# Optimization experiments

Hardware: AMD Instinct MI355X
Metric: run time of the kernel (lower is better)

## Reference

```python
import jax, jax.numpy as jnp
import numpy as np

B, S, SV = 4, 2048, 50
QF = KF = VF = E = 1024
SCALE = np.float32(np.power(KF, 0.5))


def setup_inputs() -> dict:
    key = jax.random.key(0)
    ks = jax.random.split(key, 8)
    s = 0.02
    return {
        "Q": jax.random.normal(ks[0], (B, S, QF), dtype=jnp.float32),
        "K": jax.random.normal(ks[1], (B, S, KF), dtype=jnp.float32),
        "V": jax.random.normal(ks[2], (B, SV, VF), dtype=jnp.float32),
        # weights stored [in, out] so forward is x @ W (== torch Linear with weight.T)
        "W_Q": jax.random.normal(ks[3], (QF, E), dtype=jnp.float32) * s,
        "W_K": jax.random.normal(ks[4], (KF, E), dtype=jnp.float32) * s,
        "W_v": jax.random.normal(ks[5], (E, E), dtype=jnp.float32) * s,
        "W_vq": jax.random.normal(ks[6], (SV, E), dtype=jnp.float32) * s,
        "W_vk": jax.random.normal(ks[7], (SV, E), dtype=jnp.float32) * s,
    }


def reference(Q, K, V, W_Q, W_K, W_v, W_vq, W_vk):
    # mode == 'mode2', dropout=None (inference path)
    q = jnp.tanh(Q) @ W_Q          # [B,S,E]
    k = jnp.tanh(K) @ W_K          # [B,S,E]
    v = jnp.tanh(V) @ W_v          # [B,SV,E]

    qk = jnp.einsum('bse,bte->bst', q, k) / SCALE   # [B,S,S]
    vq = jnp.einsum('bse,bve->bsv', q, v) / SCALE   # [B,S,SV]
    vk = jnp.einsum('bse,bve->bsv', k, v) / SCALE   # [B,S,SV]

    f = jax.nn.softmax(qk, axis=-1)                 # [B,S,S]
    g = 1.0 - f

    q2 = jnp.einsum('bst,bte->bse', f, q) + vq @ W_vq
    k2 = jnp.einsum('bst,bte->bse', g, k) + vk @ W_vk

    Q_out = jnp.einsum('bst,bte->bse', f, q2)
    K_out = jnp.einsum('bst,bte->bse', g, k2)
    return (Q_out, K_out, f)
```

## Files before the change

### kernel.cpp

```cpp
#include <hip/hip_runtime.h>
#include <cstdint>
#include <cstddef>

typedef __bf16 bf16_t;
typedef __bf16 bf16x4 __attribute__((ext_vector_type(4)));
typedef __bf16 bf16x8 __attribute__((ext_vector_type(8)));
typedef float floatx4 __attribute__((ext_vector_type(4)));

#define B_ 4
#define S_ 2048
#define E_ 1024
#define SV_ 50
#define SVP_ 64
#define BSE_ ((long)B_ * S_ * E_)

__device__ __forceinline__ void async_copy16(const bf16_t* g, bf16_t* l) {
  __builtin_amdgcn_global_load_lds(
      (const __attribute__((address_space(1))) void*)g,
      (__attribute__((address_space(3))) void*)l, 16, 0, 0);
}

__global__ __launch_bounds__(256) void tanh2_k(const float* __restrict__ Q,
                                               const float* __restrict__ Kin,
                                               bf16_t* __restrict__ out) {
  long i4 = ((long)blockIdx.x * 256 + threadIdx.x) * 4;
  const long n = (long)B_ * S_ * E_;
  const float* src = (i4 < n) ? (Q + i4) : (Kin + (i4 - n));
  float4 x = *(const float4*)src;
  bf16x4 o;
  o[0] = (bf16_t)tanhf(x.x);
  o[1] = (bf16_t)tanhf(x.y);
  o[2] = (bf16_t)tanhf(x.z);
  o[3] = (bf16_t)tanhf(x.w);
  *(bf16x4*)&out[i4] = o;
}

__global__ __launch_bounds__(256) void tanh_vpad_k(const float* __restrict__ V,
                                                   bf16_t* __restrict__ out) {
  int i = blockIdx.x * 256 + threadIdx.x;
  int e = i & 1023, r = (i >> 10) & 63, b = i >> 16;
  float v = 0.f;
  if (r < SV_) v = tanhf(V[((long)(b * SV_ + r) << 10) + e]);
  out[i] = (bf16_t)v;
}

__global__ __launch_bounds__(256) void transp_cast3_k(const float* __restrict__ W0,
                                                      const float* __restrict__ W1,
                                                      const float* __restrict__ W2,
                                                      bf16_t* __restrict__ out,
                                                      int K, int N, int Kp) {
  __shared__ float tile[32][33];
  const float* W = (blockIdx.z == 0) ? W0 : (blockIdx.z == 1) ? W1 : W2;
  bf16_t* o = out + (long)blockIdx.z * N * Kp;
  int k0 = blockIdx.y * 32, n0 = blockIdx.x * 32;
  int tx = threadIdx.x, ty = threadIdx.y;
#pragma unroll
  for (int s2 = 0; s2 < 4; ++s2) {
    int kk = ty + s2 * 8;
    float v = 0.f;
    if (k0 + kk < K && n0 + tx < N) v = W[(long)(k0 + kk) * N + n0 + tx];
    tile[kk][tx] = v;
  }
  __syncthreads();
#pragma unroll
  for (int s2 = 0; s2 < 4; ++s2) {
    int nn = ty + s2 * 8;
    if (n0 + nn < N && k0 + tx < Kp)
      o[(long)(n0 + nn) * Kp + k0 + tx] = (bf16_t)tile[tx][nn];
  }
}

__global__ __launch_bounds__(256) void transp_bf16_k(const bf16_t* __restrict__ in,
                                                     long inRow, long inBatch,
                                                     bf16_t* __restrict__ out,
                                                     long outRow, long outBatch) {
  __shared__ bf16_t tile[32][33];
  int r0 = blockIdx.y * 32, c0 = blockIdx.x * 32;
  int tx = threadIdx.x, ty = threadIdx.y;
  long ib = (long)blockIdx.z * inBatch;
  long ob = (long)blockIdx.z * outBatch;
#pragma unroll
  for (int s2 = 0; s2 < 4; ++s2)
    tile[ty + s2 * 8][tx] = in[ib + (long)(r0 + ty + s2 * 8) * inRow + c0 + tx];
  __syncthreads();
#pragma unroll
  for (int s2 = 0; s2 < 4; ++s2)
    out[ob + (long)(c0 + ty + s2 * 8) * outRow + r0 + tx] = tile[tx][ty + s2 * 8];
}

__global__ __launch_bounds__(256) void colsum_part_k(const bf16_t* __restrict__ X,
                                                     long rowStride, long batchStride,
                                                     float* __restrict__ part) {
  int e = blockIdx.x * 256 + threadIdx.x;
  int chunk = blockIdx.y, b = blockIdx.z;
  const bf16_t* p = X + (long)b * batchStride + (long)chunk * 256 * rowStride + e;
  float s = 0.f;
#pragma unroll 8
  for (int t = 0; t < 256; ++t) s += (float)p[(long)t * rowStride];
  part[((long)b * 8 + chunk) * E_ + e] = s;
}

__global__ __launch_bounds__(256) void colsum_fin_k(const float* __restrict__ part,
                                                    float* __restrict__ out) {
  int e = blockIdx.x * 256 + threadIdx.x;
  int b = blockIdx.y;
  float s = 0.f;
#pragma unroll
  for (int c = 0; c < 8; ++c) s += part[((long)b * 8 + c) * E_ + e];
  out[(long)b * E_ + e] = s;
}

__global__ __launch_bounds__(256) void softmax_row_k(bf16_t* __restrict__ fb,
                                                     float* __restrict__ Fout) {
  long off = ((long)blockIdx.y * S_ + blockIdx.x) * S_;
  int t = threadIdx.x;
  bf16x8 xb = *(const bf16x8*)&fb[off + 8 * t];
  float x[8];
#pragma unroll
  for (int i = 0; i < 8; ++i) x[i] = (float)xb[i];
  float mx = fmaxf(fmaxf(fmaxf(x[0], x[1]), fmaxf(x[2], x[3])),
                   fmaxf(fmaxf(x[4], x[5]), fmaxf(x[6], x[7])));
#pragma unroll
  for (int s = 32; s >= 1; s >>= 1) mx = fmaxf(mx, __shfl_xor(mx, s));
  __shared__ float red[4];
  int wv = t >> 6;
  if ((t & 63) == 0) red[wv] = mx;
  __syncthreads();
  mx = fmaxf(fmaxf(red[0], red[1]), fmaxf(red[2], red[3]));
  float e[8];
  float sum = 0.f;
#pragma unroll
  for (int i = 0; i < 8; ++i) {
    e[i] = __expf(x[i] - mx);
    sum += e[i];
  }
#pragma unroll
  for (int s = 32; s >= 1; s >>= 1) sum += __shfl_xor(sum, s);
  __shared__ float red2[4];
  if ((t & 63) == 0) red2[wv] = sum;
  __syncthreads();
  float inv = 1.0f / ((red2[0] + red2[1]) + (red2[2] + red2[3]));
  bf16x8 ob;
#pragma unroll
  for (int i = 0; i < 8; ++i) {
    e[i] *= inv;
    ob[i] = (bf16_t)e[i];
  }
  *(float4*)&Fout[off + 8 * t] = make_float4(e[0], e[1], e[2], e[3]);
  *(float4*)&Fout[off + 8 * t + 4] = make_float4(e[4], e[5], e[6], e[7]);
  *(bf16x8*)&fb[off + 8 * t] = ob;
}

__global__ __launch_bounds__(256) void gemm_vqk_k(const bf16_t* __restrict__ qkb,
                                                  const bf16_t* __restrict__ vb,
                                                  bf16_t* __restrict__ vqkf) {
  __shared__ __align__(16) bf16_t As[64 * 64];
  __shared__ __align__(16) bf16_t Bs[64 * 64];
  const int zz = blockIdx.z;
  const int sel = zz >> 2;
  const int b = zz & 3;
  const bf16_t* Ab = qkb + (long)sel * BSE_ + (long)b * S_ * E_;
  const bf16_t* Bb = vb + (long)b * SVP_ * E_;
  bf16_t* outB = vqkf + ((long)b * 2 + sel) * ((long)S_ * SVP_);
  const int t = threadIdx.x;
  const int lane = t & 63;
  const int wave = t >> 6;
  const int wm = (wave & 1) * 32;
  const int wn = (wave >> 1) * 32;
  const long rowBase = (long)blockIdx.y * 64;

  floatx4 acc[2][2];
#pragma unroll
  for (int i = 0; i < 2; ++i)
#pragma unroll
    for (int j = 0; j < 2; ++j) acc[i][j] = {0.f, 0.f, 0.f, 0.f};

  const int sr = t >> 3;
  const int sc = (t & 7) * 8;
  for (int k0 = 0; k0 < E_; k0 += 64) {
#pragma unroll
    for (int p = 0; p < 2; ++p) {
      int r = p * 32 + sr;
      *(uint4*)&As[r * 64 + sc] = *(const uint4*)&Ab[(rowBase + r) * E_ + k0 + sc];
      *(uint4*)&Bs[r * 64 + sc] = *(const uint4*)&Bb[(long)r * E_ + k0 + sc];
    }
    __syncthreads();
#pragma unroll
    for (int ks = 0; ks < 64; ks += 32) {
      const int fr = lane & 15;
      const int fk = ks + ((lane >> 4) << 3);
      bf16x8 a0 = *(const bf16x8*)&As[(wm + fr) * 64 + fk];
      bf16x8 a1 = *(const bf16x8*)&As[(wm + 16 + fr) * 64 + fk];
      bf16x8 b0 = *(const bf16x8*)&Bs[(wn + fr) * 64 + fk];
      bf16x8 b1 = *(const bf16x8*)&Bs[(wn + 16 + fr) * 64 + fk];
      acc[0][0] = __builtin_amdgcn_mfma_f32_16x16x32_bf16(a0, b0, acc[0][0], 0, 0, 0);
      acc[0][1] = __builtin_amdgcn_mfma_f32_16x16x32_bf16(a0, b1, acc[0][1], 0, 0, 0);
      acc[1][0] = __builtin_amdgcn_mfma_f32_16x16x32_bf16(a1, b0, acc[1][0], 0, 0, 0);
      acc[1][1] = __builtin_amdgcn_mfma_f32_16x16x32_bf16(a1, b1, acc[1][1], 0, 0, 0);
    }
    __syncthreads();
  }

  const int cr = lane & 15;
  const int rq = (lane >> 4) * 4;
  const float alpha = sel ? -1.f / 32.f : 1.f / 32.f;
#pragma unroll
  for (int i = 0; i < 2; ++i)
#pragma unroll
    for (int j = 0; j < 2; ++j)
#pragma unroll
      for (int r = 0; r < 4; ++r) {
        long row = rowBase + wm + i * 16 + rq + r;
        int col = wn + j * 16 + cr;
        outB[row * SVP_ + col] = (bf16_t)(alpha * acc[i][j][r]);
      }
}

__global__ __launch_bounds__(256) void gemm_fused_k(
    const bf16_t* __restrict__ A1, long sA1,
    const bf16_t* __restrict__ B1, long sB1,
    int N, int K1,
    const bf16_t* __restrict__ A2q, const bf16_t* __restrict__ A2k, long sA2,
    const bf16_t* __restrict__ B2,
    float alpha, int negSplit, const float* __restrict__ colVec, long sV,
    float* __restrict__ outFa, bf16_t* __restrict__ outBa, int lda, long sOa,
    float* __restrict__ outFb, bf16_t* __restrict__ outBb, int ldb, long sOb,
    int capZ, int capM) {
  __shared__ __align__(16) bf16_t As[128 * 64];
  __shared__ __align__(16) bf16_t Bs[128 * 64];
  const int t = threadIdx.x;
  const int lane = t & 63;
  const int wave = t >> 6;
  const int wm = (wave & 1) * 64;
  const int wn = (wave >> 1) * 64;
  const long b = blockIdx.z;
  const long rowBase = (long)blockIdx.y * 128;
  const long colBase = (long)blockIdx.x * 128;
  if ((int)b >= capZ && rowBase >= capM) return;
  const bf16_t* Ab = A1 + b * sA1;
  const bf16_t* Bb = B1 + b * sB1;

  floatx4 acc[4][4];
#pragma unroll
  for (int i = 0; i < 4; ++i)
#pragma unroll
    for (int j = 0; j < 4; ++j) acc[i][j] = {0.f, 0.f, 0.f, 0.f};

  const int srow = lane >> 3;
  const int schunk = (lane & 7) ^ srow;
  const bf16_t* aG[4];
  const bf16_t* bG[4];
  bf16_t* aL[4];
  bf16_t* bL[4];
#pragma unroll
  for (int i = 0; i < 4; ++i) {
    int r = wave * 32 + i * 8;
    aG[i] = Ab + (rowBase + r + srow) * (long)K1 + schunk * 8;
    bG[i] = Bb + (colBase + r + srow) * (long)K1 + schunk * 8;
    aL[i] = &As[r * 64];
    bL[i] = &Bs[r * 64];
  }

  const int fr = lane & 15;
  const int hi = lane >> 4;
  int aoff[4], boff[4];
#pragma unroll
  for (int i = 0; i < 4; ++i) {
    aoff[i] = (wm + i * 16 + fr) * 64 + ((hi ^ (fr & 7)) * 8);
    boff[i] = (wn + i * 16 + fr) * 64 + ((hi ^ (fr & 7)) * 8);
  }

  for (int k0 = 0; k0 < K1; k0 += 64) {
#pragma unroll
    for (int i = 0; i < 4; ++i) {
      async_copy16(aG[i] + k0, aL[i]);
      async_copy16(bG[i] + k0, bL[i]);
    }
    __syncthreads();
#pragma unroll
    for (int ks = 0; ks < 64; ks += 32) {
      bf16x8 af[4], bf[4];
#pragma unroll
      for (int i = 0; i < 4; ++i) af[i] = *(const bf16x8*)&As[aoff[i] ^ ks];
#pragma unroll
      for (int i = 0; i < 4; ++i) bf[i] = *(const bf16x8*)&Bs[boff[i] ^ ks];
#pragma unroll
      for (int i = 0; i < 4; ++i)
#pragma unroll
        for (int j = 0; j < 4; ++j)
          acc[i][j] =
              __builtin_amdgcn_mfma_f32_16x16x32_bf16(af[i], bf[j], acc[i][j], 0, 0, 0);
    }
    __syncthreads();
  }

  if (A2q) {
    const bf16_t* A2 = (colBase >= negSplit) ? A2k : A2q;
    const bf16_t* A2b = A2 + b * sA2;
#pragma unroll
    for (int i = 0; i < 4; ++i) {
      int r = wave * 32 + i * 8;
      async_copy16(A2b + (rowBase + r + srow) * 64 + schunk * 8, aL[i]);
      async_copy16(B2 + (colBase + r + srow) * 64 + schunk * 8, bL[i]);
    }
    __syncthreads();
#pragma unroll
    for (int ks = 0; ks < 64; ks += 32) {
      bf16x8 af[4], bf[4];
#pragma unroll
      for (int i = 0; i < 4; ++i) af[i] = *(const bf16x8*)&As[aoff[i] ^ ks];
#pragma unroll
      for (int i = 0; i < 4; ++i) bf[i] = *(const bf16x8*)&Bs[boff[i] ^ ks];
#pragma unroll
      for (int i = 0; i < 4; ++i)
#pragma unroll
        for (int j = 0; j < 4; ++j)
          acc[i][j] =
              __builtin_amdgcn_mfma_f32_16x16x32_bf16(af[i], bf[j], acc[i][j], 0, 0, 0);
    }
    __syncthreads();
  }

  const int cr = lane & 15;
  const int rq = hi * 4;
  const bool neg = (colBase >= negSplit);
  const float* cv = colVec ? (colVec + b * sV + (neg ? colBase - negSplit : colBase))
                           : nullptr;
  float* oF = neg ? outFb : outFa;
  bf16_t* oB = neg ? outBb : outBa;
  const int ld = neg ? ldb : lda;
  const long sO = neg ? sOb : sOa;
  const long cb0 = neg ? (long)(colBase - negSplit) : colBase;
#pragma unroll
  for (int i = 0; i < 4; ++i)
#pragma unroll
    for (int j = 0; j < 4; ++j)
#pragma unroll
      for (int r = 0; r < 4; ++r) {
        long row = rowBase + wm + i * 16 + rq + r;
        int c = wn + j * 16 + cr;
        float v = alpha * acc[i][j][r];
        if (neg) v = cv[c] - v;
        long o = b * sO + row * (long)ld + cb0 + c;
        if (oF) oF[o] = v;
        if (oB) oB[o] = (bf16_t)v;
      }
}

extern "C" void kernel_launch(void* const* d_in, const int* in_sizes, int n_in,
                              void* d_out, int out_size, void* d_ws, size_t ws_size,
                              hipStream_t stream) {
  const float* Q = (const float*)d_in[0];
  const float* Kin = (const float*)d_in[1];
  const float* V = (const float*)d_in[2];
  const float* W_Q = (const float*)d_in[3];
  const float* W_K = (const float*)d_in[4];
  const float* W_v = (const float*)d_in[5];
  const float* W_vq = (const float*)d_in[6];
  const float* W_vk = (const float*)d_in[7];

  float* Qout = (float*)d_out;
  float* Kout = Qout + (long)B_ * S_ * E_;
  float* Fout = Kout + (long)B_ * S_ * E_;

  char* w = (char*)d_ws;
  auto alloc = [&](size_t bytes) {
    char* p = w;
    w += (bytes + 255) & ~(size_t)255;
    return p;
  };
  const long BSE = BSE_;
  bf16_t* WQKt = (bf16_t*)alloc((size_t)2 * 2 * E_ * E_);
  bf16_t* WVt = (bf16_t*)alloc((size_t)2 * E_ * E_);
  bf16_t* Wv2T = (bf16_t*)alloc((size_t)2 * 2 * E_ * SVP_);
  bf16_t* QtKt = (bf16_t*)alloc((size_t)2 * 2 * BSE);
  bf16_t* Vt = (bf16_t*)alloc((size_t)2 * B_ * SVP_ * E_);
  bf16_t* qkb = (bf16_t*)alloc((size_t)2 * 2 * BSE);
  bf16_t* vb = (bf16_t*)alloc((size_t)2 * B_ * SVP_ * E_);
  bf16_t* qkT = (bf16_t*)alloc((size_t)2 * (long)B_ * 2 * E_ * S_);
  bf16_t* fb = (bf16_t*)alloc((size_t)2 * (long)B_ * S_ * S_);
  bf16_t* vqkf = (bf16_t*)alloc((size_t)2 * (long)B_ * 2 * S_ * SVP_);
  bf16_t* q2k2 = (bf16_t*)alloc((size_t)2 * (long)B_ * S_ * 2 * E_);
  bf16_t* q2k2T = (bf16_t*)alloc((size_t)2 * (long)B_ * 2 * E_ * S_);
  float* part = (float*)alloc((size_t)4 * B_ * 8 * E_);
  float* ck = (float*)alloc((size_t)4 * B_ * E_);
  float* ck2 = (float*)alloc((size_t)4 * B_ * E_);

  bf16_t* qb = qkb;
  bf16_t* kb = qkb + BSE;

  dim3 blk256(256);
  dim3 blk32x8(32, 8);

  transp_cast3_k<<<dim3(32, 32, 3), blk32x8, 0, stream>>>(W_Q, W_K, W_v, WQKt,
                                                          E_, E_, E_);
  transp_cast3_k<<<dim3(32, 2, 2), blk32x8, 0, stream>>>(W_vq, W_vk, W_vq, Wv2T,
                                                         SV_, E_, SVP_);

  tanh2_k<<<dim3((unsigned)(2 * BSE / 1024)), blk256, 0, stream>>>(Q, Kin, QtKt);
  tanh_vpad_k<<<dim3(B_ * SVP_ * E_ / 256), blk256, 0, stream>>>(V, Vt);

  gemm_fused_k<<<dim3(E_ / 128, B_ * S_ / 128, 3), blk256, 0, stream>>>(
      QtKt, BSE, WQKt, (long)E_ * E_, E_, E_,
      nullptr, nullptr, 0, nullptr, 1.f, E_, nullptr, 0,
      nullptr, qkb, E_, BSE, nullptr, nullptr, 0, 0,
      2, B_ * SVP_);

  transp_bf16_k<<<dim3(E_ / 32, S_ / 32, B_), blk32x8, 0, stream>>>(
      qb, E_, (long)S_ * E_, qkT, S_, (long)2 * E_ * S_);
  transp_bf16_k<<<dim3(E_ / 32, S_ / 32, B_), blk32x8, 0, stream>>>(
      kb, E_, (long)S_ * E_, qkT + (long)E_ * S_, S_, (long)2 * E_ * S_);

  gemm_fused_k<<<dim3(S_ / 128, S_ / 128, B_), blk256, 0, stream>>>(
      qb, (long)S_ * E_, kb, (long)S_ * E_, S_, E_,
      nullptr, nullptr, 0, nullptr, 1.f / 32.f, S_, nullptr, 0,
      nullptr, fb, S_, (long)S_ * S_, nullptr, nullptr, 0, 0,
      9999, 0);
  softmax_row_k<<<dim3(S_, B_), blk256, 0, stream>>>(fb, Fout);

  colsum_part_k<<<dim3(E_ / 256, 8, B_), blk256, 0, stream>>>(kb, E_, (long)S_ * E_, part);
  colsum_fin_k<<<dim3(E_ / 256, B_), blk256, 0, stream>>>(part, ck);

  gemm_vqk_k<<<dim3(1, S_ / 64, 2 * B_), blk256, 0, stream>>>(qkb, vb, vqkf);

  gemm_fused_k<<<dim3(2 * E_ / 128, S_ / 128, B_), blk256, 0, stream>>>(
      fb, (long)S_ * S_, qkT, (long)2 * E_ * S_, 2 * E_, S_,
      vqkf, vqkf + (long)S_ * SVP_, (long)2 * S_ * SVP_, Wv2T,
      1.f, E_, ck, E_,
      nullptr, q2k2, 2 * E_, (long)S_ * 2 * E_,
      nullptr, q2k2 + E_, 2 * E_, (long)S_ * 2 * E_,
      9999, 0);

  transp_bf16_k<<<dim3(E_ / 32, S_ / 32, B_), blk32x8, 0, stream>>>(
      q2k2, 2 * E_, (long)S_ * 2 * E_, q2k2T, S_, (long)2 * E_ * S_);
  transp_bf16_k<<<dim3(E_ / 32, S_ / 32, B_), blk32x8, 0, stream>>>(
      q2k2 + E_, 2 * E_, (long)S_ * 2 * E_, q2k2T + (long)E_ * S_, S_, (long)2 * E_ * S_);

  colsum_part_k<<<dim3(E_ / 256, 8, B_), blk256, 0, stream>>>(
      q2k2 + E_, 2 * E_, (long)S_ * 2 * E_, part);
  colsum_fin_k<<<dim3(E_ / 256, B_), blk256, 0, stream>>>(part, ck2);

  gemm_fused_k<<<dim3(2 * E_ / 128, S_ / 128, B_), blk256, 0, stream>>>(
      fb, (long)S_ * S_, q2k2T, (long)2 * E_ * S_, 2 * E_, S_,
      nullptr, nullptr, 0, nullptr,
      1.f, E_, ck2, E_,
      Qout, nullptr, E_, (long)S_ * E_,
      Kout, nullptr, E_, (long)S_ * E_,
      9999, 0);
}
```

Baseline: 636.7 us.

## Double-buffer GEMM LDS tiles with async prefetch and merge transpose launches

The shared GEMM kernel now keeps two LDS buffers per operand and prefetches the tile two steps ahead with async global-to-LDS copies. It waits on partial vmcnt counts, so loads overlap the MFMA work instead of stalling on a full sync every K step. The extra A2/B2 tail step is folded into the same pipeline. Pairs of transpose launches are also merged into one launch. LDS use doubles to 64KB per block, which may reduce occupancy.

```diff
diff --git a/kernel.cpp b/kernel.cpp
--- a/kernel.cpp
+++ b/kernel.cpp
@@ -70,15 +70,18 @@
   }
 }
 
-__global__ __launch_bounds__(256) void transp_bf16_k(const bf16_t* __restrict__ in,
-                                                     long inRow, long inBatch,
-                                                     bf16_t* __restrict__ out,
-                                                     long outRow, long outBatch) {
+__global__ __launch_bounds__(256) void transp2_bf16_k(const bf16_t* __restrict__ in,
+                                                      long selIn, long inRow,
+                                                      long inBatch,
+                                                      bf16_t* __restrict__ out,
+                                                      long selOut, long outRow,
+                                                      long outBatch) {
   __shared__ bf16_t tile[32][33];
   int r0 = blockIdx.y * 32, c0 = blockIdx.x * 32;
   int tx = threadIdx.x, ty = threadIdx.y;
-  long ib = (long)blockIdx.z * inBatch;
-  long ob = (long)blockIdx.z * outBatch;
+  int half = blockIdx.z & 1, bz = blockIdx.z >> 1;
+  long ib = (long)bz * inBatch + (long)half * selIn;
+  long ob = (long)bz * outBatch + (long)half * selOut;
 #pragma unroll
   for (int s2 = 0; s2 < 4; ++s2)
     tile[ty + s2 * 8][tx] = in[ib + (long)(r0 + ty + s2 * 8) * inRow + c0 + tx];
@@ -226,8 +229,8 @@
     float* __restrict__ outFa, bf16_t* __restrict__ outBa, int lda, long sOa,
     float* __restrict__ outFb, bf16_t* __restrict__ outBb, int ldb, long sOb,
     int capZ, int capM) {
-  __shared__ __align__(16) bf16_t As[128 * 64];
-  __shared__ __align__(16) bf16_t Bs[128 * 64];
+  __shared__ __align__(16) bf16_t As[2 * 128 * 64];
+  __shared__ __align__(16) bf16_t Bs[2 * 128 * 64];
   const int t = threadIdx.x;
   const int lane = t & 63;
   const int wave = t >> 6;
@@ -250,15 +253,13 @@
   const int schunk = (lane & 7) ^ srow;
   const bf16_t* aG[4];
   const bf16_t* bG[4];
-  bf16_t* aL[4];
-  bf16_t* bL[4];
+  int lofs[4];
 #pragma unroll
   for (int i = 0; i < 4; ++i) {
     int r = wave * 32 + i * 8;
     aG[i] = Ab + (rowBase + r + srow) * (long)K1 + schunk * 8;
     bG[i] = Bb + (colBase + r + srow) * (long)K1 + schunk * 8;
-    aL[i] = &As[r * 64];
-    bL[i] = &Bs[r * 64];
+    lofs[i] = r * 64;
   }
 
   const int fr = lane & 15;
@@ -270,55 +271,61 @@
     boff[i] = (wn + i * 16 + fr) * 64 + ((hi ^ (fr & 7)) * 8);
   }
 
-  for (int k0 = 0; k0 < K1; k0 += 64) {
-#pragma unroll
-    for (int i = 0; i < 4; ++i) {
-      async_copy16(aG[i] + k0, aL[i]);
-      async_copy16(bG[i] + k0, bL[i]);
+  const int nK1 = K1 >> 6;
+  const int nt = nK1 + (A2q ? 1 : 0);
+
+  auto stage = [&](int buf, int kt) {
+    const int bo = buf * (128 * 64);
+    if (kt < nK1) {
+      const long k0 = (long)kt * 64;
+#pragma unroll
+      for (int i = 0; i < 4; ++i) {
+        async_copy16(aG[i] + k0, &As[bo + lofs[i]]);
+        async_copy16(bG[i] + k0, &Bs[bo + lofs[i]]);
+      }
+    } else {
+      const bf16_t* A2 = (colBase >= negSplit) ? A2k : A2q;
+      const bf16_t* A2b = A2 + b * sA2;
+#pragma unroll
+      for (int i = 0; i < 4; ++i) {
+        int r = wave * 32 + i * 8;
+        async_copy16(A2b + (rowBase + r + srow) * 64 + schunk * 8, &As[bo + lofs[i]]);
+        async_copy16(B2 + (colBase + r + srow) * 64 + schunk * 8, &Bs[bo + lofs[i]]);
+      }
     }
-    __syncthreads();
+  };
+
+  stage(0, 0);
+  if (nt > 1) stage(1, 1);
+
+  for (int kt = 0; kt < nt; ++kt) {
+    if (kt < nt - 1)
+      asm volatile("s_waitcnt vmcnt(8)" ::: "memory");
+    else
+      asm volatile("s_waitcnt vmcnt(0)" ::: "memory");
+    __builtin_amdgcn_s_barrier();
+    __builtin_amdgcn_sched_barrier(0);
+    const int bo = (kt & 1) * (128 * 64);
+    __builtin_amdgcn_s_setprio(1);
 #pragma unroll
     for (int ks = 0; ks < 64; ks += 32) {
-      bf16x8 af[4], bf[4];
-#pragma unroll
-      for (int i = 0; i < 4; ++i) af[i] = *(const bf16x8*)&As[aoff[i] ^ ks];
-#pragma unroll
-      for (int i = 0; i < 4; ++i) bf[i] = *(const bf16x8*)&Bs[boff[i] ^ ks];
+      bf16x8 af[4], bfr[4];
+#pragma unroll
+      for (int i = 0; i < 4; ++i) af[i] = *(const bf16x8*)&As[bo + (aoff[i] ^ ks)];
+#pragma unroll
+      for (int i = 0; i < 4; ++i) bfr[i] = *(const bf16x8*)&Bs[bo + (boff[i] ^ ks)];
 #pragma unroll
       for (int i = 0; i < 4; ++i)
 #pragma unroll
         for (int j = 0; j < 4; ++j)
           acc[i][j] =
-              __builtin_amdgcn_mfma_f32_16x16x32_bf16(af[i], bf[j], acc[i][j], 0, 0, 0);
+              __builtin_amdgcn_mfma_f32_16x16x32_bf16(af[i], bfr[j], acc[i][j], 0, 0, 0);
     }
-    __syncthreads();
-  }
-
-  if (A2q) {
-    const bf16_t* A2 = (colBase >= negSplit) ? A2k : A2q;
-    const bf16_t* A2b = A2 + b * sA2;
-#pragma unroll
-    for (int i = 0; i < 4; ++i) {
-      int r = wave * 32 + i * 8;
-      async_copy16(A2b + (rowBase + r + srow) * 64 + schunk * 8, aL[i]);
-      async_copy16(B2 + (colBase + r + srow) * 64 + schunk * 8, bL[i]);
-    }
-    __syncthreads();
-#pragma unroll
-    for (int ks = 0; ks < 64; ks += 32) {
-      bf16x8 af[4], bf[4];
-#pragma unroll
-      for (int i = 0; i < 4; ++i) af[i] = *(const bf16x8*)&As[aoff[i] ^ ks];
-#pragma unroll
-      for (int i = 0; i < 4; ++i) bf[i] = *(const bf16x8*)&Bs[boff[i] ^ ks];
-#pragma unroll
-      for (int i = 0; i < 4; ++i)
-#pragma unroll
-        for (int j = 0; j < 4; ++j)
-          acc[i][j] =
-              __builtin_amdgcn_mfma_f32_16x16x32_bf16(af[i], bf[j], acc[i][j], 0, 0, 0);
-    }
-    __syncthreads();
+    __builtin_amdgcn_s_setprio(0);
+    __builtin_amdgcn_sched_barrier(0);
+    __builtin_amdgcn_s_barrier();
+    __builtin_amdgcn_sched_barrier(0);
+    if (kt + 2 < nt) stage(kt & 1, kt + 2);
   }
 
   const int cr = lane & 15;
@@ -406,10 +413,8 @@
       nullptr, qkb, E_, BSE, nullptr, nullptr, 0, 0,
       2, B_ * SVP_);
 
-  transp_bf16_k<<<dim3(E_ / 32, S_ / 32, B_), blk32x8, 0, stream>>>(
-      qb, E_, (long)S_ * E_, qkT, S_, (long)2 * E_ * S_);
-  transp_bf16_k<<<dim3(E_ / 32, S_ / 32, B_), blk32x8, 0, stream>>>(
-      kb, E_, (long)S_ * E_, qkT + (long)E_ * S_, S_, (long)2 * E_ * S_);
+  transp2_bf16_k<<<dim3(E_ / 32, S_ / 32, 2 * B_), blk32x8, 0, stream>>>(
+      qkb, BSE, E_, (long)S_ * E_, qkT, (long)E_ * S_, S_, (long)2 * E_ * S_);
 
   gemm_fused_k<<<dim3(S_ / 128, S_ / 128, B_), blk256, 0, stream>>>(
       qb, (long)S_ * E_, kb, (long)S_ * E_, S_, E_,
@@ -431,10 +436,9 @@
       nullptr, q2k2 + E_, 2 * E_, (long)S_ * 2 * E_,
       9999, 0);
 
-  transp_bf16_k<<<dim3(E_ / 32, S_ / 32, B_), blk32x8, 0, stream>>>(
-      q2k2, 2 * E_, (long)S_ * 2 * E_, q2k2T, S_, (long)2 * E_ * S_);
-  transp_bf16_k<<<dim3(E_ / 32, S_ / 32, B_), blk32x8, 0, stream>>>(
-      q2k2 + E_, 2 * E_, (long)S_ * 2 * E_, q2k2T + (long)E_ * S_, S_, (long)2 * E_ * S_);
+  transp2_bf16_k<<<dim3(E_ / 32, S_ / 32, 2 * B_), blk32x8, 0, stream>>>(
+      q2k2, E_, 2 * E_, (long)S_ * 2 * E_, q2k2T, (long)E_ * S_, S_,
+      (long)2 * E_ * S_);
 
   colsum_part_k<<<dim3(E_ / 256, 8, B_), blk256, 0, stream>>>(
       q2k2 + E_, 2 * E_, (long)S_ * 2 * E_, part);
```

New measurement: 604.3 us. -5.1%, faster.
